# Kernel tuning notes

Hardware: AMD Instinct MI355X
Metric: run time of the kernel (lower is better)

Reference implementation:

```python
import jax, jax.numpy as jnp
import numpy as np

B, S, V, E, H, C = 64, 1024, 50000, 256, 256, 20
BOUND_P = 0.05  # ~20-word sentences


def setup_inputs() -> dict:
    key = jax.random.key(0)
    k1, k2, k3, k4, k5, k6, k7 = jax.random.split(key, 7)
    tokens = jax.random.randint(k1, (B, S), 2, V)
    is_bound = jax.random.uniform(k2, (B, S)) < BOUND_P
    batch_x = jnp.where(is_bound, 1, tokens)
    batch_x = batch_x.at[:, S - 1].set(1)  # force final sentence boundary
    batch_lens = jnp.full((B,), S, dtype=jnp.int32)
    emb = jax.random.normal(k3, (V, E), dtype=jnp.float32) * 0.1
    W1 = jax.random.normal(k4, (E, H), dtype=jnp.float32) * (1.0 / np.sqrt(E))
    b1 = jnp.zeros((H,), dtype=jnp.float32)
    W2 = jax.random.normal(k5, (H, H), dtype=jnp.float32) * (1.0 / np.sqrt(H))
    b2 = jnp.zeros((H,), dtype=jnp.float32)
    W3 = jax.random.normal(k6, (H, C), dtype=jnp.float32) * (1.0 / np.sqrt(H))
    b3 = jnp.zeros((C,), dtype=jnp.float32)
    return {"batch_x": batch_x, "batch_lens": batch_lens, "emb": emb,
            "W1": W1, "b1": b1, "W2": W2, "b2": b2, "W3": W3, "b3": b3}


def reference(batch_x, batch_lens, emb, W1, b1, W2, b2, W3, b3):
    # word embedding gather: (B,S,E)
    word_embed = emb[batch_x]
    # word2sent nn layer (position-wise fc + tanh), dropout=identity (eval)
    h = jnp.tanh(jnp.einsum('bse,eh->bsh', word_embed, W1) + b1)
    # sentence segmentation: token id 1 marks end of sentence (inclusive)
    is_bound = (batch_x == 1)
    bcum = jnp.cumsum(is_bound.astype(jnp.int32), axis=1)
    local_id = bcum - is_bound.astype(jnp.int32)  # sentence index of each token
    doc_lens = bcum[:, -1]                        # sentences per doc
    valid = local_id < doc_lens[:, None]          # tokens after last boundary dropped
    seg = jnp.arange(B, dtype=jnp.int32)[:, None] * S + local_id
    seg = jnp.where(valid, seg, B * S)            # dump invalid tokens in spare bucket
    h_flat = h.reshape(B * S, H)
    sums = jax.ops.segment_sum(h_flat, seg.reshape(-1), num_segments=B * S + 1)[:B * S]
    cnts = jax.ops.segment_sum(valid.astype(h.dtype).reshape(-1), seg.reshape(-1),
                               num_segments=B * S + 1)[:B * S]
    # word2sent mean pooling (padded/empty slots -> 0, matching F.pad)
    sent_embed = (sums / jnp.maximum(cnts, 1.0)[:, None]).reshape(B, S, H)
    # sent2doc nn layer + mean pooling over valid sentences
    sent_hidden = jnp.tanh(jnp.einsum('bsh,hk->bsk', sent_embed, W2) + b2)
    sent_valid = (jnp.arange(S)[None, :] < doc_lens[:, None]).astype(h.dtype)
    doc_embed = jnp.einsum('bsk,bs->bk', sent_hidden, sent_valid) / doc_lens[:, None].astype(h.dtype)
    # classifier head
    cat_space = doc_embed @ W3 + b3
    return jax.nn.log_softmax(cat_space, axis=-1)
```

## Files before the change

### kernel.cpp

```cpp
#include <hip/hip_runtime.h>
#include <hip/hip_bf16.h>
#include <cstdint>
#include <cstddef>

#define NB 64
#define NS 1024
#define NV 50000
#define NE 256
#define NH 256
#define NC 20
#define SMAX2 128
#define MAXSEG 25

typedef short bf16x8 __attribute__((ext_vector_type(8)));
typedef float f32x4 __attribute__((ext_vector_type(4)));

#define WS_W1T    0
#define WS_W2T    131072
#define WS_STARTS 262144
#define WS_LENS   524544
#define WS_PREF   524800
#define WS_PBLK   526848
#define WS_SH     13634048

__device__ inline float bf2f(unsigned short u) {
    return __uint_as_float(((unsigned int)u) << 16);
}
__device__ inline unsigned short f2bf(float f) {
    unsigned int x = __float_as_uint(f);
    unsigned int r = (x + 0x7FFFu + ((x >> 16) & 1u)) >> 16;
    return (unsigned short)r;
}
__device__ inline float fast_tanh(float x) {
    float e = __expf(2.f * x);
    return 1.f - 2.f / (e + 1.f);
}

__global__ void setup_kernel(const float* __restrict__ W1, const float* __restrict__ W2,
                             const int* __restrict__ x,
                             unsigned short* __restrict__ W1T, unsigned short* __restrict__ W2T,
                             int* __restrict__ starts, int* __restrict__ lens,
                             int* __restrict__ pref) {
    int blk = blockIdx.x;
    if (blk < 512) {
        int idx = blk * 256 + threadIdx.x;
        if (idx < NE * NH) {
            int h = idx >> 8, e = idx & 255;
            W1T[idx] = f2bf(W1[e * NH + h]);
        } else {
            int i = idx - NE * NH;
            int j = i >> 8, k = i & 255;
            W2T[i] = f2bf(W2[k * NH + j]);
        }
    } else {
        if (threadIdx.x >= 64) return;
        int b = blk - 512;
        int lane = threadIdx.x;
        const int* row = x + b * NS;
        int* st = starts + b * (NS + 1);
        if (lane == 0) st[0] = 0;
        int cnt = 0;
        for (int it = 0; it < NS / 64; ++it) {
            if ((it & 1) == 0 && lane == 0) pref[b * 8 + (it >> 1)] = cnt;
            int s = it * 64 + lane;
            bool isb = (row[s] == 1);
            unsigned long long bal = __ballot(isb);
            int pre = __popcll(bal & ((1ull << lane) - 1ull));
            if (isb) st[cnt + pre + 1] = s + 1;
            cnt += __popcll(bal);
        }
        if (lane == 0) lens[b] = cnt;
    }
}

__global__ __launch_bounds__(256, 2) void gemm1_kernel(
    const int* __restrict__ batch_x, const float* __restrict__ emb,
    const unsigned short* __restrict__ W1T, const float* __restrict__ b1,
    float* __restrict__ pblk)
{
    __shared__ unsigned short As[2][16][264];
    __shared__ unsigned short Hs[16][264];
    __shared__ float segsum[MAXSEG][256];
    __shared__ int sidtab[128];
    __shared__ int nb_sh;

    int tid = threadIdx.x;
    int lane = tid & 63;
    int w = tid >> 6;
    int lr = lane & 15;
    int g = lane >> 4;
    int kb0 = g * 8;
    int base = blockIdx.x * 128;

    for (int s = tid; s < MAXSEG * 256; s += 256) (&segsum[0][0])[s] = 0.f;

    if (w == 0) {
        int cnt = 0;
        #pragma unroll
        for (int c = 0; c < 2; ++c) {
            int t = c * 64 + lane;
            bool isb = (batch_x[base + t] == 1);
            unsigned long long bal = __ballot(isb);
            int pre = __popcll(bal & ((1ull << lane) - 1ull));
            int sid = cnt + pre;
            sidtab[t] = sid < MAXSEG ? sid : MAXSEG - 1;
            cnt += __popcll(bal);
        }
        if (lane == 0) nb_sh = cnt < MAXSEG ? cnt : MAXSEG - 1;
    }

    bf16x8 Bf[32];
    #pragma unroll
    for (int ks = 0; ks < 8; ++ks)
        #pragma unroll
        for (int n = 0; n < 4; ++n)
            Bf[ks * 4 + n] = *reinterpret_cast<const bf16x8*>(
                W1T + (size_t)(w * 64 + n * 16 + lr) * NE + ks * 32 + kb0);
    float bb[4];
    #pragma unroll
    for (int n = 0; n < 4; ++n) bb[n] = b1[w * 64 + n * 16 + lr];

    float4 gr[4];
    #pragma unroll
    for (int i = 0; i < 4; ++i) {
        int f = tid + i * 256;
        int row = f >> 6, c4 = (f & 63) * 4;
        int xv = batch_x[base + row];
        gr[i] = *reinterpret_cast<const float4*>(emb + (size_t)xv * NE + c4);
    }
    #pragma unroll
    for (int i = 0; i < 4; ++i) {
        int f = tid + i * 256;
        int row = f >> 6, c4 = (f & 63) * 4;
        ushort4 u;
        u.x = f2bf(gr[i].x); u.y = f2bf(gr[i].y); u.z = f2bf(gr[i].z); u.w = f2bf(gr[i].w);
        *reinterpret_cast<ushort4*>(&As[0][row][c4]) = u;
    }

    int cur_sid = 0;
    float running = 0.f;

    for (int t = 0; t < 8; ++t) {
        __syncthreads();
        int cur = t & 1;

        if (t + 1 < 8) {
            #pragma unroll
            for (int i = 0; i < 4; ++i) {
                int f = tid + i * 256;
                int row = f >> 6, c4 = (f & 63) * 4;
                int xv = batch_x[base + (t + 1) * 16 + row];
                gr[i] = *reinterpret_cast<const float4*>(emb + (size_t)xv * NE + c4);
            }
        }

        f32x4 acc[4];
        #pragma unroll
        for (int n = 0; n < 4; ++n) acc[n] = (f32x4){0.f, 0.f, 0.f, 0.f};
        #pragma unroll
        for (int ks = 0; ks < 8; ++ks) {
            bf16x8 a = *reinterpret_cast<const bf16x8*>(&As[cur][lr][ks * 32 + kb0]);
            #pragma unroll
            for (int n = 0; n < 4; ++n)
                acc[n] = __builtin_amdgcn_mfma_f32_16x16x32_bf16(a, Bf[ks * 4 + n], acc[n], 0, 0, 0);
        }

        #pragma unroll
        for (int n = 0; n < 4; ++n) {
            int col = w * 64 + n * 16 + lr;
            #pragma unroll
            for (int j = 0; j < 4; ++j)
                Hs[g * 4 + j][col] = f2bf(fast_tanh(acc[n][j] + bb[n]));
        }
        __syncthreads();

        int rowbase = t * 16;
        #pragma unroll
        for (int r = 0; r < 16; ++r) {
            int s = sidtab[rowbase + r];
            if (s != cur_sid) { segsum[cur_sid][tid] += running; running = 0.f; cur_sid = s; }
            running += bf2f(Hs[r][tid]);
        }

        if (t + 1 < 8) {
            #pragma unroll
            for (int i = 0; i < 4; ++i) {
                int f = tid + i * 256;
                int row = f >> 6, c4 = (f & 63) * 4;
                ushort4 u;
                u.x = f2bf(gr[i].x); u.y = f2bf(gr[i].y); u.z = f2bf(gr[i].z); u.w = f2bf(gr[i].w);
                *reinterpret_cast<ushort4*>(&As[cur ^ 1][row][c4]) = u;
            }
        }
    }
    segsum[cur_sid][tid] += running;

    int nb = nb_sh;
    for (int s = 0; s <= nb; ++s)
        pblk[((size_t)blockIdx.x * MAXSEG + s) * NH + tid] = segsum[s][tid];
}

__global__ __launch_bounds__(256, 2) void sgemm_kernel(
    const float* __restrict__ pblk, const int* __restrict__ starts,
    const int* __restrict__ lens, const int* __restrict__ pref,
    const unsigned short* __restrict__ W2T, const float* __restrict__ b2,
    unsigned short* __restrict__ shbuf)
{
    int b = blockIdx.y;
    int i0 = blockIdx.x * 16;
    int L = lens[b];
    if (i0 >= L) return;

    int tid = threadIdx.x;
    int lane = tid & 63;
    int w = tid >> 6;
    int lr = lane & 15;
    int g = lane >> 4;
    int kb0 = g * 8;

    __shared__ unsigned short ms[16][264];

    bf16x8 Bf[32];
    #pragma unroll
    for (int ks = 0; ks < 8; ++ks)
        #pragma unroll
        for (int n = 0; n < 4; ++n)
            Bf[ks * 4 + n] = *reinterpret_cast<const bf16x8*>(
                W2T + (size_t)(w * 64 + n * 16 + lr) * NH + ks * 32 + kb0);
    float bb[4];
    #pragma unroll
    for (int n = 0; n < 4; ++n) bb[n] = b2[w * 64 + n * 16 + lr];

    const int* st = starts + b * (NS + 1);
    for (int s = 0; s < 16; ++s) {
        int i = i0 + s;
        float m = 0.f;
        if (i < L) {
            int s0 = st[i], e0 = st[i + 1];
            int tb1 = (e0 - 1) >> 7;
            float sum = 0.f;
            for (int tb = s0 >> 7; tb <= tb1; ++tb) {
                int blk = b * 8 + tb;
                sum += pblk[((size_t)blk * MAXSEG + (i - pref[blk])) * NH + tid];
            }
            m = sum / (float)(e0 - s0);
        }
        ms[s][tid] = f2bf(m);
    }
    __syncthreads();

    f32x4 acc[4];
    #pragma unroll
    for (int n = 0; n < 4; ++n) acc[n] = (f32x4){0.f, 0.f, 0.f, 0.f};
    #pragma unroll
    for (int ks = 0; ks < 8; ++ks) {
        bf16x8 a = *reinterpret_cast<const bf16x8*>(&ms[lr][ks * 32 + kb0]);
        #pragma unroll
        for (int n = 0; n < 4; ++n)
            acc[n] = __builtin_amdgcn_mfma_f32_16x16x32_bf16(a, Bf[ks * 4 + n], acc[n], 0, 0, 0);
    }

    #pragma unroll
    for (int n = 0; n < 4; ++n) {
        int col = w * 64 + n * 16 + lr;
        #pragma unroll
        for (int j = 0; j < 4; ++j) {
            int srow = i0 + g * 4 + j;
            if (srow < L)
                shbuf[((size_t)b * SMAX2 + srow) * NH + col] = f2bf(tanhf(acc[n][j] + bb[n]));
        }
    }
}

__global__ __launch_bounds__(1024) void doc_kernel(
    const unsigned short* __restrict__ shbuf, const int* __restrict__ lens,
    const float* __restrict__ W3, const float* __restrict__ b3,
    float* __restrict__ out)
{
    int b = blockIdx.x;
    int tid = threadIdx.x;
    int j = tid & 255;
    int q = tid >> 8;
    int L = lens[b];

    __shared__ float part[4][256];
    __shared__ float d[256];
    __shared__ float cat[NC];

    const unsigned short* sp = shbuf + (size_t)b * SMAX2 * NH + j;
    float a0 = 0.f, a1 = 0.f;
    int i = q;
    for (; i + 8 <= L; i += 8) {
        a0 += bf2f(sp[(size_t)i * NH]);
        a1 += bf2f(sp[(size_t)(i + 4) * NH]);
    }
    for (; i < L; i += 4) a0 += bf2f(sp[(size_t)i * NH]);
    part[q][j] = a0 + a1;
    __syncthreads();

    if (tid < 256)
        d[j] = ((part[0][j] + part[1][j]) + (part[2][j] + part[3][j])) / (float)L;
    __syncthreads();

    if (tid < NC) {
        float a = b3[tid];
        #pragma unroll 8
        for (int k = 0; k < NH; ++k) a += d[k] * W3[k * NC + tid];
        cat[tid] = a;
    }
    __syncthreads();

    if (tid == 0) {
        float mx = -1e30f;
        for (int c = 0; c < NC; ++c) mx = fmaxf(mx, cat[c]);
        float se = 0.f;
        for (int c = 0; c < NC; ++c) se += expf(cat[c] - mx);
        float lse = logf(se) + mx;
        for (int c = 0; c < NC; ++c) out[b * NC + c] = cat[c] - lse;
    }
}

extern "C" void kernel_launch(void* const* d_in, const int* in_sizes, int n_in,
                              void* d_out, int out_size, void* d_ws, size_t ws_size,
                              hipStream_t stream) {
    const int*   batch_x = (const int*)d_in[0];
    const float* emb = (const float*)d_in[2];
    const float* W1  = (const float*)d_in[3];
    const float* b1  = (const float*)d_in[4];
    const float* W2  = (const float*)d_in[5];
    const float* b2  = (const float*)d_in[6];
    const float* W3  = (const float*)d_in[7];
    const float* b3  = (const float*)d_in[8];
    float* out = (float*)d_out;

    char* ws = (char*)d_ws;
    unsigned short* W1T   = (unsigned short*)(ws + WS_W1T);
    unsigned short* W2T   = (unsigned short*)(ws + WS_W2T);
    int*            starts= (int*)(ws + WS_STARTS);
    int*            lens  = (int*)(ws + WS_LENS);
    int*            pref  = (int*)(ws + WS_PREF);
    float*          pblk  = (float*)(ws + WS_PBLK);
    unsigned short* shbuf = (unsigned short*)(ws + WS_SH);

    hipLaunchKernelGGL(setup_kernel, dim3(512 + NB), dim3(256), 0, stream,
                       W1, W2, batch_x, W1T, W2T, starts, lens, pref);
    hipLaunchKernelGGL(gemm1_kernel, dim3((NB * NS) / 128), dim3(256), 0, stream,
                       batch_x, emb, W1T, b1, pblk);
    hipLaunchKernelGGL(sgemm_kernel, dim3(SMAX2 / 16, NB), dim3(256), 0, stream,
                       pblk, starts, lens, pref, W2T, b2, shbuf);
    hipLaunchKernelGGL(doc_kernel, dim3(NB), dim3(1024), 0, stream,
                       shbuf, lens, W3, b3, out);
}
```

Before: 75.27 us.

## Fuse sentence GEMM with doc pooling and widen gemm1 to 512 threads

The sentence-level GEMM, doc mean pooling and classifier head are merged into one kernel per document. Each block loops over 16-sentence tiles, double-buffers the mean tile in shared memory and accumulates tanh column sums in registers, so the intermediate shbuf round-trip and one launch go away. gemm1 now runs 512 threads (8 waves of 32 columns each, launch bounds 512,4), which halves per-thread weight registers. It also drops the shared-memory segment-sum array and writes each finished segment sum straight to pblk. The trade-off is less parallelism in the fused stage (only 64 blocks, looping serially over tiles). Direct writes also overwrite rather than accumulate if segments ever collide at the clamped MAXSEG index.

```diff
diff --git a/kernel.cpp b/kernel.cpp
--- a/kernel.cpp
+++ b/kernel.cpp
@@ -9,7 +9,6 @@
 #define NE 256
 #define NH 256
 #define NC 20
-#define SMAX2 128
 #define MAXSEG 25
 
 typedef short bf16x8 __attribute__((ext_vector_type(8)));
@@ -21,7 +20,6 @@
 #define WS_LENS   524544
 #define WS_PREF   524800
 #define WS_PBLK   526848
-#define WS_SH     13634048
 
 __device__ inline float bf2f(unsigned short u) {
     return __uint_as_float(((unsigned int)u) << 16);
@@ -73,16 +71,14 @@
     }
 }
 
-__global__ __launch_bounds__(256, 2) void gemm1_kernel(
+__global__ __launch_bounds__(512, 4) void gemm1_kernel(
     const int* __restrict__ batch_x, const float* __restrict__ emb,
     const unsigned short* __restrict__ W1T, const float* __restrict__ b1,
     float* __restrict__ pblk)
 {
     __shared__ unsigned short As[2][16][264];
     __shared__ unsigned short Hs[16][264];
-    __shared__ float segsum[MAXSEG][256];
     __shared__ int sidtab[128];
-    __shared__ int nb_sh;
 
     int tid = threadIdx.x;
     int lane = tid & 63;
@@ -91,8 +87,6 @@
     int g = lane >> 4;
     int kb0 = g * 8;
     int base = blockIdx.x * 128;
-
-    for (int s = tid; s < MAXSEG * 256; s += 256) (&segsum[0][0])[s] = 0.f;
 
     if (w == 0) {
         int cnt = 0;
@@ -106,31 +100,30 @@
             sidtab[t] = sid < MAXSEG ? sid : MAXSEG - 1;
             cnt += __popcll(bal);
         }
-        if (lane == 0) nb_sh = cnt < MAXSEG ? cnt : MAXSEG - 1;
-    }
-
-    bf16x8 Bf[32];
+    }
+
+    bf16x8 Bf[16];
     #pragma unroll
     for (int ks = 0; ks < 8; ++ks)
         #pragma unroll
-        for (int n = 0; n < 4; ++n)
-            Bf[ks * 4 + n] = *reinterpret_cast<const bf16x8*>(
-                W1T + (size_t)(w * 64 + n * 16 + lr) * NE + ks * 32 + kb0);
-    float bb[4];
-    #pragma unroll
-    for (int n = 0; n < 4; ++n) bb[n] = b1[w * 64 + n * 16 + lr];
-
-    float4 gr[4];
-    #pragma unroll
-    for (int i = 0; i < 4; ++i) {
-        int f = tid + i * 256;
+        for (int n = 0; n < 2; ++n)
+            Bf[ks * 2 + n] = *reinterpret_cast<const bf16x8*>(
+                W1T + (size_t)(w * 32 + n * 16 + lr) * NE + ks * 32 + kb0);
+    float bb[2];
+    #pragma unroll
+    for (int n = 0; n < 2; ++n) bb[n] = b1[w * 32 + n * 16 + lr];
+
+    float4 gr[2];
+    #pragma unroll
+    for (int i = 0; i < 2; ++i) {
+        int f = tid + i * 512;
         int row = f >> 6, c4 = (f & 63) * 4;
         int xv = batch_x[base + row];
         gr[i] = *reinterpret_cast<const float4*>(emb + (size_t)xv * NE + c4);
     }
     #pragma unroll
-    for (int i = 0; i < 4; ++i) {
-        int f = tid + i * 256;
+    for (int i = 0; i < 2; ++i) {
+        int f = tid + i * 512;
         int row = f >> 6, c4 = (f & 63) * 4;
         ushort4 u;
         u.x = f2bf(gr[i].x); u.y = f2bf(gr[i].y); u.z = f2bf(gr[i].z); u.w = f2bf(gr[i].w);
@@ -146,46 +139,51 @@
 
         if (t + 1 < 8) {
             #pragma unroll
-            for (int i = 0; i < 4; ++i) {
-                int f = tid + i * 256;
+            for (int i = 0; i < 2; ++i) {
+                int f = tid + i * 512;
                 int row = f >> 6, c4 = (f & 63) * 4;
                 int xv = batch_x[base + (t + 1) * 16 + row];
                 gr[i] = *reinterpret_cast<const float4*>(emb + (size_t)xv * NE + c4);
             }
         }
 
-        f32x4 acc[4];
-        #pragma unroll
-        for (int n = 0; n < 4; ++n) acc[n] = (f32x4){0.f, 0.f, 0.f, 0.f};
+        f32x4 acc[2];
+        #pragma unroll
+        for (int n = 0; n < 2; ++n) acc[n] = (f32x4){0.f, 0.f, 0.f, 0.f};
         #pragma unroll
         for (int ks = 0; ks < 8; ++ks) {
             bf16x8 a = *reinterpret_cast<const bf16x8*>(&As[cur][lr][ks * 32 + kb0]);
             #pragma unroll
-            for (int n = 0; n < 4; ++n)
-                acc[n] = __builtin_amdgcn_mfma_f32_16x16x32_bf16(a, Bf[ks * 4 + n], acc[n], 0, 0, 0);
-        }
-
-        #pragma unroll
-        for (int n = 0; n < 4; ++n) {
-            int col = w * 64 + n * 16 + lr;
+            for (int n = 0; n < 2; ++n)
+                acc[n] = __builtin_amdgcn_mfma_f32_16x16x32_bf16(a, Bf[ks * 2 + n], acc[n], 0, 0, 0);
+        }
+
+        #pragma unroll
+        for (int n = 0; n < 2; ++n) {
+            int col = w * 32 + n * 16 + lr;
             #pragma unroll
             for (int j = 0; j < 4; ++j)
                 Hs[g * 4 + j][col] = f2bf(fast_tanh(acc[n][j] + bb[n]));
         }
         __syncthreads();
 
-        int rowbase = t * 16;
-        #pragma unroll
-        for (int r = 0; r < 16; ++r) {
-            int s = sidtab[rowbase + r];
-            if (s != cur_sid) { segsum[cur_sid][tid] += running; running = 0.f; cur_sid = s; }
-            running += bf2f(Hs[r][tid]);
+        if (tid < 256) {
+            int rowbase = t * 16;
+            #pragma unroll
+            for (int r = 0; r < 16; ++r) {
+                int s = sidtab[rowbase + r];
+                if (s != cur_sid) {
+                    pblk[((size_t)blockIdx.x * MAXSEG + cur_sid) * NH + tid] = running;
+                    running = 0.f; cur_sid = s;
+                }
+                running += bf2f(Hs[r][tid]);
+            }
         }
 
         if (t + 1 < 8) {
             #pragma unroll
-            for (int i = 0; i < 4; ++i) {
-                int f = tid + i * 256;
+            for (int i = 0; i < 2; ++i) {
+                int f = tid + i * 512;
                 int row = f >> 6, c4 = (f & 63) * 4;
                 ushort4 u;
                 u.x = f2bf(gr[i].x); u.y = f2bf(gr[i].y); u.z = f2bf(gr[i].z); u.w = f2bf(gr[i].w);
@@ -193,24 +191,19 @@
             }
         }
     }
-    segsum[cur_sid][tid] += running;
-
-    int nb = nb_sh;
-    for (int s = 0; s <= nb; ++s)
-        pblk[((size_t)blockIdx.x * MAXSEG + s) * NH + tid] = segsum[s][tid];
-}
-
-__global__ __launch_bounds__(256, 2) void sgemm_kernel(
+    if (tid < 256)
+        pblk[((size_t)blockIdx.x * MAXSEG + cur_sid) * NH + tid] = running;
+}
+
+__global__ __launch_bounds__(256, 2) void sentdoc_kernel(
     const float* __restrict__ pblk, const int* __restrict__ starts,
     const int* __restrict__ lens, const int* __restrict__ pref,
     const unsigned short* __restrict__ W2T, const float* __restrict__ b2,
-    unsigned short* __restrict__ shbuf)
+    const float* __restrict__ W3, const float* __restrict__ b3,
+    float* __restrict__ out)
 {
-    int b = blockIdx.y;
-    int i0 = blockIdx.x * 16;
+    int b = blockIdx.x;
     int L = lens[b];
-    if (i0 >= L) return;
-
     int tid = threadIdx.x;
     int lane = tid & 63;
     int w = tid >> 6;
@@ -218,7 +211,10 @@
     int g = lane >> 4;
     int kb0 = g * 8;
 
-    __shared__ unsigned short ms[16][264];
+    __shared__ unsigned short ms[2][16][264];
+    __shared__ float dcol[256];
+    __shared__ float dvec[256];
+    __shared__ float cat[NC];
 
     bf16x8 Bf[32];
     #pragma unroll
@@ -231,81 +227,69 @@
     #pragma unroll
     for (int n = 0; n < 4; ++n) bb[n] = b2[w * 64 + n * 16 + lr];
 
+    float colsum[4] = {0.f, 0.f, 0.f, 0.f};
     const int* st = starts + b * (NS + 1);
-    for (int s = 0; s < 16; ++s) {
-        int i = i0 + s;
-        float m = 0.f;
-        if (i < L) {
-            int s0 = st[i], e0 = st[i + 1];
-            int tb1 = (e0 - 1) >> 7;
-            float sum = 0.f;
-            for (int tb = s0 >> 7; tb <= tb1; ++tb) {
-                int blk = b * 8 + tb;
-                sum += pblk[((size_t)blk * MAXSEG + (i - pref[blk])) * NH + tid];
-            }
-            m = sum / (float)(e0 - s0);
-        }
-        ms[s][tid] = f2bf(m);
+    int ntiles = (L + 15) >> 4;
+
+    for (int t = 0; t < ntiles; ++t) {
+        int i0 = t * 16;
+        for (int s = 0; s < 16; ++s) {
+            int i = i0 + s;
+            float m = 0.f;
+            if (i < L) {
+                int s0 = st[i], e0 = st[i + 1];
+                int tb1 = (e0 - 1) >> 7;
+                float sum = 0.f;
+                for (int tb = s0 >> 7; tb <= tb1; ++tb) {
+                    int blk = b * 8 + tb;
+                    sum += pblk[((size_t)blk * MAXSEG + (i - pref[blk])) * NH + tid];
+                }
+                m = sum / (float)(e0 - s0);
+            }
+            ms[t & 1][s][tid] = f2bf(m);
+        }
+        __syncthreads();
+
+        f32x4 acc[4];
+        #pragma unroll
+        for (int n = 0; n < 4; ++n) acc[n] = (f32x4){0.f, 0.f, 0.f, 0.f};
+        #pragma unroll
+        for (int ks = 0; ks < 8; ++ks) {
+            bf16x8 a = *reinterpret_cast<const bf16x8*>(&ms[t & 1][lr][ks * 32 + kb0]);
+            #pragma unroll
+            for (int n = 0; n < 4; ++n)
+                acc[n] = __builtin_amdgcn_mfma_f32_16x16x32_bf16(a, Bf[ks * 4 + n], acc[n], 0, 0, 0);
+        }
+
+        #pragma unroll
+        for (int n = 0; n < 4; ++n) {
+            float v = 0.f;
+            #pragma unroll
+            for (int j = 0; j < 4; ++j) {
+                int srow = i0 + g * 4 + j;
+                float hv = tanhf(acc[n][j] + bb[n]);
+                v += (srow < L) ? hv : 0.f;
+            }
+            colsum[n] += v;
+        }
+    }
+
+    #pragma unroll
+    for (int n = 0; n < 4; ++n) {
+        float v = colsum[n];
+        v += __shfl_xor(v, 16, 64);
+        v += __shfl_xor(v, 32, 64);
+        if (g == 0) dcol[w * 64 + n * 16 + lr] = v;
     }
     __syncthreads();
 
-    f32x4 acc[4];
-    #pragma unroll
-    for (int n = 0; n < 4; ++n) acc[n] = (f32x4){0.f, 0.f, 0.f, 0.f};
-    #pragma unroll
-    for (int ks = 0; ks < 8; ++ks) {
-        bf16x8 a = *reinterpret_cast<const bf16x8*>(&ms[lr][ks * 32 + kb0]);
-        #pragma unroll
-        for (int n = 0; n < 4; ++n)
-            acc[n] = __builtin_amdgcn_mfma_f32_16x16x32_bf16(a, Bf[ks * 4 + n], acc[n], 0, 0, 0);
-    }
-
-    #pragma unroll
-    for (int n = 0; n < 4; ++n) {
-        int col = w * 64 + n * 16 + lr;
-        #pragma unroll
-        for (int j = 0; j < 4; ++j) {
-            int srow = i0 + g * 4 + j;
-            if (srow < L)
-                shbuf[((size_t)b * SMAX2 + srow) * NH + col] = f2bf(tanhf(acc[n][j] + bb[n]));
-        }
-    }
-}
-
-__global__ __launch_bounds__(1024) void doc_kernel(
-    const unsigned short* __restrict__ shbuf, const int* __restrict__ lens,
-    const float* __restrict__ W3, const float* __restrict__ b3,
-    float* __restrict__ out)
-{
-    int b = blockIdx.x;
-    int tid = threadIdx.x;
-    int j = tid & 255;
-    int q = tid >> 8;
-    int L = lens[b];
-
-    __shared__ float part[4][256];
-    __shared__ float d[256];
-    __shared__ float cat[NC];
-
-    const unsigned short* sp = shbuf + (size_t)b * SMAX2 * NH + j;
-    float a0 = 0.f, a1 = 0.f;
-    int i = q;
-    for (; i + 8 <= L; i += 8) {
-        a0 += bf2f(sp[(size_t)i * NH]);
-        a1 += bf2f(sp[(size_t)(i + 4) * NH]);
-    }
-    for (; i < L; i += 4) a0 += bf2f(sp[(size_t)i * NH]);
-    part[q][j] = a0 + a1;
-    __syncthreads();
-
-    if (tid < 256)
-        d[j] = ((part[0][j] + part[1][j]) + (part[2][j] + part[3][j])) / (float)L;
+    dvec[tid] = dcol[tid] / (float)L;
     __syncthreads();
 
     if (tid < NC) {
         float a = b3[tid];
         #pragma unroll 8
-        for (int k = 0; k < NH; ++k) a += d[k] * W3[k * NC + tid];
+        for (int k = 0; k < NH; ++k) a += dvec[k] * W3[k * NC + tid];
         cat[tid] = a;
     }
     __syncthreads();
@@ -340,14 +324,11 @@
     int*            lens  = (int*)(ws + WS_LENS);
     int*            pref  = (int*)(ws + WS_PREF);
     float*          pblk  = (float*)(ws + WS_PBLK);
-    unsigned short* shbuf = (unsigned short*)(ws + WS_SH);
 
     hipLaunchKernelGGL(setup_kernel, dim3(512 + NB), dim3(256), 0, stream,
                        W1, W2, batch_x, W1T, W2T, starts, lens, pref);
-    hipLaunchKernelGGL(gemm1_kernel, dim3((NB * NS) / 128), dim3(256), 0, stream,
+    hipLaunchKernelGGL(gemm1_kernel, dim3((NB * NS) / 128), dim3(512), 0, stream,
                        batch_x, emb, W1T, b1, pblk);
-    hipLaunchKernelGGL(sgemm_kernel, dim3(SMAX2 / 16, NB), dim3(256), 0, stream,
-                       pblk, starts, lens, pref, W2T, b2, shbuf);
-    hipLaunchKernelGGL(doc_kernel, dim3(NB), dim3(1024), 0, stream,
-                       shbuf, lens, W3, b3, out);
-}
+    hipLaunchKernelGGL(sentdoc_kernel, dim3(NB), dim3(256), 0, stream,
+                       pblk, starts, lens, pref, W2T, b2, W3, b3, out);
+}
```

Result: slower. 86.87 us (+15.4%).
